# Kernel optimization log

Hardware: AMD Instinct MI355X
Metric: run time of the kernel (lower is better)

## Reference

```python
import jax, jax.numpy as jnp
import numpy as np

B = 2048
ENB = 16      # enb_cnt (beams)
RBG = 32      # rbg_cnt
MAXREQ = 50   # max_req
OBS_F = 400   # Requests features = 50*8
H = 1024
OUT = ENB * RBG * (MAXREQ + 1)  # 26112
IN = OBS_F + ENB * RBG + ENB * MAXREQ  # 1712


def _linear_init(key, fan_in, fan_out):
    kw, kb = jax.random.split(key)
    lim = 1.0 / np.sqrt(fan_in)
    W = jax.random.uniform(kw, (fan_in, fan_out), jnp.float32, -lim, lim)
    b = jax.random.uniform(kb, (fan_out,), jnp.float32, -lim, lim)
    return W, b


def setup_inputs() -> dict:
    key = jax.random.key(0)
    ks = jax.random.split(key, 6)
    obs = jax.random.normal(ks[0], (B, OBS_F), jnp.float32)
    rbgMap = jax.random.randint(ks[1], (B, ENB, RBG), 0, 2).astype(jnp.float32)
    invFlag = (jax.random.randint(ks[2], (B, ENB, MAXREQ), 0, 3) - 1).astype(jnp.float32)
    W1, b1 = _linear_init(ks[3], IN, H)
    W2, b2 = _linear_init(ks[4], H, H)
    W3, b3 = _linear_init(ks[5], H, OUT)
    return {"obs": obs, "rbgMap": rbgMap, "invFlag": invFlag,
            "W1": W1, "b1": b1, "W2": W2, "b2": b2, "W3": W3, "b3": b3}


def reference(obs, rbgMap, invFlag, W1, b1, W2, b2, W3, b3):
    Bt = obs.shape[0]
    rbg_flat = rbgMap.reshape(Bt, ENB * RBG)                      # [B, E*R]
    inv = invFlag.reshape(Bt, ENB, MAXREQ)
    # am1: invFlag broadcast per-rbg -> [B, E*R, MAXREQ]
    am1 = jnp.broadcast_to(inv[:, :, None, :], (Bt, ENB, RBG, MAXREQ)).reshape(Bt, ENB * RBG, MAXREQ)
    rbg_exp = rbg_flat[:, :, None]                                 # [B, E*R, 1]
    # vectorized form of the nested loops:
    #   where am1 == -1: -> 1 if rbg==0, 0 if rbg==1; else unchanged
    am1 = jnp.where(am1 == -1.0, jnp.where(rbg_exp == 0.0, 1.0, 0.0), am1)
    # prepend never-masked no-op action column, mask = nonzero
    amask = jnp.concatenate([jnp.zeros((Bt, ENB * RBG, 1), am1.dtype), am1], axis=2) != 0
    # dense MLP on concatenated observation
    inp = jnp.concatenate([obs, rbg_flat, invFlag.reshape(Bt, -1)], axis=1)  # [B, 1712]
    h = jnp.tanh(inp @ W1 + b1)
    h = jnp.tanh(h @ W2 + b2)
    logits = (h @ W3 + b3).reshape(Bt, ENB * RBG, MAXREQ + 1)
    logits = jnp.where(amask, -jnp.inf, logits)
    return logits
```

## Files before the change

kernel.cpp:

```cpp
#include <hip/hip_runtime.h>
#include <math.h>

#define B_    2048
#define OBSF_ 400
#define H_    1024
#define IN_   1712
#define INP_  1728
#define KS1_  54
#define KSH_  32
#define OUT_  26112
#define NCOL_ 51
#define MAXQ_ 50

#define NEG_BIG (-3.0e38f)

typedef __attribute__((ext_vector_type(4))) float  floatx4;
typedef __bf16 bf16x8 __attribute__((ext_vector_type(8)));

__device__ __forceinline__ unsigned short f2b(float v) {
    unsigned u = __float_as_uint(v);
    u += 0x7FFFu + ((u >> 16) & 1u);
    return (unsigned short)(u >> 16);
}


__global__ __launch_bounds__(256)
void pack_frag(const float* __restrict__ obs,
               const float* __restrict__ rbg,
               const float* __restrict__ inv,
               unsigned short* __restrict__ P) {
    const int tid = threadIdx.x;
    const int wave = tid >> 6, lane = tid & 63;
    const int cid = blockIdx.x * 4 + wave;
    const int ks = cid % KS1_, r16 = cid / KS1_;
    const int r = r16 * 16 + (lane & 15);
    const int kb = ks * 32 + (lane >> 4) * 8;
    __attribute__((aligned(16))) unsigned short tmp[8];
    #pragma unroll
    for (int j = 0; j < 8; j++) {
        int k = kb + j;
        float v = 0.0f;
        if (k < OBSF_)            v = obs[r * OBSF_ + k];
        else if (k < OBSF_ + 512) v = rbg[r * 512 + (k - OBSF_)];
        else if (k < IN_)         v = inv[r * 800 + (k - OBSF_ - 512)];
        tmp[j] = f2b(v);
    }
    *(uint4*)(P + ((size_t)(r16 * KS1_ + ks) * 64 + lane) * 8) = *(const uint4*)tmp;
}

__global__ __launch_bounds__(256)
void transpose_frag(const float* __restrict__ W, unsigned short* __restrict__ P,
                    int K, int N, int KS) {
    __shared__ float tile[32][129];
    const int n0 = blockIdx.x * 128, k0 = blockIdx.y * 32;
    const int tid = threadIdx.x;
    const int nn = tid & 127, kk0 = tid >> 7;
    #pragma unroll
    for (int i = 0; i < 16; i++) {
        int k = k0 + kk0 + i * 2;
        float v = 0.0f;
        if (k < K) v = W[(size_t)k * N + n0 + nn];
        tile[kk0 + i * 2][nn] = v;
    }
    __syncthreads();
    const int wave = tid >> 6, lane = tid & 63;
    const int i16 = lane & 15, q = lane >> 4;
    #pragma unroll
    for (int c2 = 0; c2 < 2; c2++) {
        const int c = wave * 2 + c2;
        __attribute__((aligned(16))) unsigned short tmp[8];
        #pragma unroll
        for (int j = 0; j < 8; j++) tmp[j] = f2b(tile[q * 8 + j][c * 16 + i16]);
        *(uint4*)(P + ((size_t)(((n0 >> 4) + c) * KS + (k0 >> 5)) * 64 + lane) * 8) =
            *(const uint4*)tmp;
    }
}

template<int MT, int NT, int KS, int EPI>
__global__ __launch_bounds__(256, 2)
void gemm_frag(const unsigned short* __restrict__ Ap,
               const unsigned short* __restrict__ Bp,
               const float* __restrict__ bias,
               void* __restrict__ outv,
               const float* __restrict__ rbg,
               const float* __restrict__ inv,
               int KSo) {
    const int tid = threadIdx.x;
    const int wave = tid >> 6, lane = tid & 63;
    const int wtm = blockIdx.y * 2 + (wave >> 1);
    const int wtn = blockIdx.x * 2 + (wave & 1);
    const int m16base = wtm * MT, n16base = wtn * NT;

    const unsigned short* pa = Ap + (size_t)m16base * KS * 512 + lane * 8;
    const unsigned short* pb = Bp + (size_t)n16base * KS * 512 + lane * 8;

    floatx4 acc[MT][NT];
    #pragma unroll
    for (int i = 0; i < MT; i++)
        #pragma unroll
        for (int j = 0; j < NT; j++) acc[i][j] = (floatx4){0.f, 0.f, 0.f, 0.f};

    bf16x8 a0[MT], b0[NT], a1[MT], b1[NT];
    #define LOADA(dst, ks_)                                                    \
        _Pragma("unroll") for (int mt = 0; mt < MT; mt++)                      \
            dst[mt] = *(const bf16x8*)(pa + (size_t)mt * KS * 512 + (ks_) * 512);
    #define LOADB(dst, ks_)                                                    \
        _Pragma("unroll") for (int nt = 0; nt < NT; nt++)                      \
            dst[nt] = *(const bf16x8*)(pb + (size_t)nt * KS * 512 + (ks_) * 512);
    #define MFMA(aa, bb)                                                       \
        _Pragma("unroll") for (int mt = 0; mt < MT; mt++)                      \
            _Pragma("unroll") for (int nt = 0; nt < NT; nt++)                  \
                acc[mt][nt] = __builtin_amdgcn_mfma_f32_16x16x32_bf16(         \
                    aa[mt], bb[nt], acc[mt][nt], 0, 0, 0);

    LOADA(a0, 0); LOADB(b0, 0);
    for (int ks = 0; ks < KS; ks += 2) {
        LOADA(a1, ks + 1); LOADB(b1, ks + 1);
        MFMA(a0, b0);
        int k2 = (ks + 2 < KS) ? ks + 2 : 0;
        LOADA(a0, k2); LOADB(b0, k2);
        MFMA(a1, b1);
    }
    #undef LOADA
    #undef LOADB
    #undef MFMA

    const int quad = lane >> 4;
    #pragma unroll
    for (int nt = 0; nt < NT; nt++) {
        const int col = (n16base + nt) * 16 + (lane & 15);
        const float bv = bias[col];
        unsigned short* Hp = (unsigned short*)outv;
        const int ko = col >> 5, kb = (col >> 3) & 3, kj = col & 7;
        #pragma unroll
        for (int mt = 0; mt < MT; mt++) {
            const int m16 = m16base + mt;
            #pragma unroll
            for (int r = 0; r < 4; r++) {
                const int mlo = quad * 4 + r;
                Hp[((size_t)(m16 * KSo + ko) * 64 + (mlo | (kb << 4))) * 8 + kj] =
                    f2b(tanhf(acc[mt][nt][r] + bv));
            }
        }
    }
}

typedef __attribute__((address_space(1))) const unsigned int gu32;
typedef __attribute__((address_space(3))) unsigned int su32;
__device__ __forceinline__ void async_copy16(unsigned short* l, const unsigned short* g) {
    __builtin_amdgcn_global_load_lds((gu32*)g, (su32*)l, 16, 0, 0);
}

template<int MT, int NT, int KS>
__global__ __launch_bounds__(256, 2)
void gemm_lds(const unsigned short* __restrict__ Ap,
              const unsigned short* __restrict__ Bp,
              const float* __restrict__ bias,
              float* __restrict__ C,
              const float* __restrict__ rbg,
              const float* __restrict__ inv) {
    constexpr int ACH = 2 * MT;
    constexpr int CH  = ACH + 2 * NT;
    constexpr int CPW = CH / 4;
    static_assert(CH % 4 == 0, "chunk count must split across 4 waves");
    static_assert(CPW == 4, "vmcnt literal below assumes CPW==4");
    static_assert(KS >= 5 && (KS - 2) % 3 == 0, "main loop unrolls by 3");
    __shared__ __align__(16) unsigned short lds[3][CH][512];

    const int tid  = threadIdx.x;
    const int wave = tid >> 6, lane = tid & 63;

    const int i = blockIdx.x;
    const int xcd = i & 7, j = i >> 3;
    const int g = xcd * 408 + j;
    const int panel = g >> 4;
    const int m     = g & 15;
    const int blk_m16 = m * ACH;
    const int blk_n16 = panel * 2 * NT;

    const int rg = wave >> 1, cg = wave & 1;
    const int m16base = blk_m16 + rg * MT;
    const int n16base = blk_n16 + cg * NT;

    const int chunk0 = wave * CPW;
    const unsigned short* gb[CPW];
    #pragma unroll
    for (int q = 0; q < CPW; q++) {
        const int c = chunk0 + q;
        gb[q] = (c < ACH ? Ap + (size_t)(blk_m16 + c) * KS * 512
                         : Bp + (size_t)(blk_n16 + (c - ACH)) * KS * 512)
                + lane * 8;
    }

    floatx4 acc[MT][NT];
    #pragma unroll
    for (int a = 0; a < MT; a++)
        #pragma unroll
        for (int b = 0; b < NT; b++) acc[a][b] = (floatx4){0.f, 0.f, 0.f, 0.f};

    #define STAGE(bufi, ksv) do {                                              \
        _Pragma("unroll")                                                      \
        for (int q = 0; q < CPW; q++)                                          \
            async_copy16(&lds[bufi][chunk0 + q][0], gb[q] + (size_t)(ksv) * 512); \
    } while (0)

    #define COMPUTE(bufi) do {                                                 \
        bf16x8 af[MT], bv[NT];                                                 \
        _Pragma("unroll")                                                      \
        for (int mt = 0; mt < MT; mt++)                                        \
            af[mt] = *(const bf16x8*)&lds[bufi][rg * MT + mt][lane * 8];       \
        _Pragma("unroll")                                                      \
        for (int nt = 0; nt < NT; nt++)                                        \
            bv[nt] = *(const bf16x8*)&lds[bufi][ACH + cg * NT + nt][lane * 8]; \
        __builtin_amdgcn_s_setprio(1);                                         \
        _Pragma("unroll")                                                      \
        for (int mt = 0; mt < MT; mt++)                                        \
            _Pragma("unroll")                                                  \
            for (int nt = 0; nt < NT; nt++)                                    \
                acc[mt][nt] = __builtin_amdgcn_mfma_f32_16x16x32_bf16(         \
                    af[mt], bv[nt], acc[mt][nt], 0, 0, 0);                     \
        __builtin_amdgcn_s_setprio(0);                                         \
    } while (0)

    #define STEP(CB, NB, tv) do {                                              \
        STAGE(NB, (tv) + 2);          \
        COMPUTE(CB);                                                           \
        asm volatile("s_waitcnt vmcnt(4)" ::: "memory");   \
        __builtin_amdgcn_s_barrier();                                          \
        asm volatile("" ::: "memory");                                         \
    } while (0)

    STAGE(0, 0);
    STAGE(1, 1);
    asm volatile("s_waitcnt vmcnt(4)" ::: "memory");
    __builtin_amdgcn_s_barrier();
    asm volatile("" ::: "memory");

    #pragma unroll 1
    for (int t = 0; t < KS - 2; t += 3) {
        STEP(0, 2, t);
        STEP(1, 0, t + 1);
        STEP(2, 1, t + 2);
    }
    COMPUTE(0);
    asm volatile("s_waitcnt vmcnt(0)" ::: "memory");
    __builtin_amdgcn_s_barrier();
    asm volatile("" ::: "memory");
    COMPUTE(1);
    #undef STEP
    #undef STAGE
    #undef COMPUTE

    const int quad = lane >> 4;
    #pragma unroll
    for (int nt = 0; nt < NT; nt++) {
        const int col = (n16base + nt) * 16 + (lane & 15);
        const float bvs = bias[col];
        const int jj = col / NCOL_;
        const int qq = col - jj * NCOL_;
        const int e  = jj >> 5;
        #pragma unroll
        for (int mt = 0; mt < MT; mt++) {
            const int row0 = (m16base + mt) * 16 + quad * 4;
            #pragma unroll
            for (int r = 0; r < 4; r++) {
                const int row = row0 + r;
                float v = acc[mt][nt][r] + bvs;
                if (qq > 0) {
                    float iv = inv[(size_t)row * 800 + e * MAXQ_ + (qq - 1)];
                    if (iv == 1.0f ||
                        (iv == -1.0f && rbg[(size_t)row * 512 + jj] == 0.0f))
                        v = NEG_BIG;
                }
                __builtin_nontemporal_store(v, &C[(size_t)row * OUT_ + col]);
            }
        }
    }
}

extern "C" void kernel_launch(void* const* d_in, const int* in_sizes, int n_in,
                              void* d_out, int out_size, void* d_ws, size_t ws_size,
                              hipStream_t stream) {
    const float* obs = (const float*)d_in[0];
    const float* rbg = (const float*)d_in[1];
    const float* inv = (const float*)d_in[2];
    const float* W1  = (const float*)d_in[3];
    const float* b1  = (const float*)d_in[4];
    const float* W2  = (const float*)d_in[5];
    const float* b2  = (const float*)d_in[6];
    const float* W3  = (const float*)d_in[7];
    const float* b3  = (const float*)d_in[8];
    float* out = (float*)d_out;

    char* ws = (char*)d_ws;
    unsigned short* inpP = (unsigned short*)ws;  ws += (size_t)B_ * INP_ * 2;
    unsigned short* W1P  = (unsigned short*)ws;  ws += (size_t)H_ * INP_ * 2;
    unsigned short* W2P  = (unsigned short*)ws;  ws += (size_t)H_ * H_ * 2;
    unsigned short* W3P  = (unsigned short*)ws;  ws += (size_t)OUT_ * H_ * 2;
    unsigned short* h1P  = (unsigned short*)ws;  ws += (size_t)B_ * H_ * 2;
    unsigned short* h2P  = (unsigned short*)ws;

    pack_frag<<<dim3(KS1_ * (B_ / 16) / 4), 256, 0, stream>>>(obs, rbg, inv, inpP);

    transpose_frag<<<dim3(H_ / 128, INP_ / 32), 256, 0, stream>>>(W1, W1P, IN_, H_, KS1_);
    transpose_frag<<<dim3(H_ / 128, H_ / 32),   256, 0, stream>>>(W2, W2P, H_, H_, KSH_);
    transpose_frag<<<dim3(OUT_ / 128, H_ / 32), 256, 0, stream>>>(W3, W3P, H_, OUT_, KSH_);

    gemm_frag<2, 2, KS1_, 0><<<dim3(H_ / 64, B_ / 64), 256, 0, stream>>>(
        inpP, W1P, b1, h1P, nullptr, nullptr, KSH_);
    gemm_frag<2, 2, KSH_, 0><<<dim3(H_ / 64, B_ / 64), 256, 0, stream>>>(
        h1P, W2P, b2, h2P, nullptr, nullptr, KSH_);
    gemm_lds<4, 4, KSH_><<<dim3(16 * (OUT_ / 128)), 256, 0, stream>>>(
        h2P, W3P, b3, out, rbg, inv);
}
```

Baseline: 577.1 us.

## Load B operand straight to registers, stage only A through LDS

The output GEMM kernel now feeds the B (weight) fragments from global memory directly into double-buffered registers, one k-step ahead. Only the A tiles still go through the triple-buffered LDS ring, which shrinks LDS per block, and the launch bounds are raised to three blocks per CU. The main loop is unrolled by six to rotate the register buffers, and the vmcnt waits are recounted for the extra loads. The aim is to cut LDS traffic and ds_reads for B and raise occupancy. The cost is that each B fragment is fetched twice from global/L2, once per row-group wave, and register pressure goes up.

```diff
diff --git a/kernel.cpp b/kernel.cpp
--- a/kernel.cpp
+++ b/kernel.cpp
@@ -152,7 +152,7 @@
 }
 
 template<int MT, int NT, int KS>
-__global__ __launch_bounds__(256, 2)
+__global__ __launch_bounds__(256, 3)
 void gemm_lds(const unsigned short* __restrict__ Ap,
               const unsigned short* __restrict__ Bp,
               const float* __restrict__ bias,
@@ -160,12 +160,10 @@
               const float* __restrict__ rbg,
               const float* __restrict__ inv) {
     constexpr int ACH = 2 * MT;
-    constexpr int CH  = ACH + 2 * NT;
-    constexpr int CPW = CH / 4;
-    static_assert(CH % 4 == 0, "chunk count must split across 4 waves");
-    static_assert(CPW == 4, "vmcnt literal below assumes CPW==4");
-    static_assert(KS >= 5 && (KS - 2) % 3 == 0, "main loop unrolls by 3");
-    __shared__ __align__(16) unsigned short lds[3][CH][512];
+    constexpr int CPW = ACH / 4;
+    static_assert(CPW == 2 && NT == 4, "vmcnt literals assume 2 stage + 4 B loads");
+    static_assert(KS % 6 == 2, "prologue 2 + 6k main + tail 2");
+    __shared__ __align__(16) unsigned short lds[3][ACH][512];
 
     const int tid  = threadIdx.x;
     const int wave = tid >> 6, lane = tid & 63;
@@ -182,73 +180,86 @@
     const int m16base = blk_m16 + rg * MT;
     const int n16base = blk_n16 + cg * NT;
 
-    const int chunk0 = wave * CPW;
-    const unsigned short* gb[CPW];
-    #pragma unroll
-    for (int q = 0; q < CPW; q++) {
-        const int c = chunk0 + q;
-        gb[q] = (c < ACH ? Ap + (size_t)(blk_m16 + c) * KS * 512
-                         : Bp + (size_t)(blk_n16 + (c - ACH)) * KS * 512)
-                + lane * 8;
-    }
+    const unsigned short* ga[CPW];
+    #pragma unroll
+    for (int q = 0; q < CPW; q++)
+        ga[q] = Ap + (size_t)(blk_m16 + wave * CPW + q) * KS * 512 + lane * 8;
+    const unsigned short* pb[NT];
+    #pragma unroll
+    for (int nt = 0; nt < NT; nt++)
+        pb[nt] = Bp + (size_t)(n16base + nt) * KS * 512 + lane * 8;
 
     floatx4 acc[MT][NT];
     #pragma unroll
     for (int a = 0; a < MT; a++)
         #pragma unroll
         for (int b = 0; b < NT; b++) acc[a][b] = (floatx4){0.f, 0.f, 0.f, 0.f};
+
+    bf16x8 bb0[NT], bb1[NT];
 
     #define STAGE(bufi, ksv) do {                                              \
         _Pragma("unroll")                                                      \
         for (int q = 0; q < CPW; q++)                                          \
-            async_copy16(&lds[bufi][chunk0 + q][0], gb[q] + (size_t)(ksv) * 512); \
+            async_copy16(&lds[bufi][wave * CPW + q][0],                        \
+                         ga[q] + (size_t)(ksv) * 512);                         \
     } while (0)
 
-    #define COMPUTE(bufi) do {                                                 \
-        bf16x8 af[MT], bv[NT];                                                 \
+    #define LOADB(dst, ksv) do {                                               \
+        _Pragma("unroll")                                                      \
+        for (int nt = 0; nt < NT; nt++)                                        \
+            dst[nt] = *(const bf16x8*)(pb[nt] + (size_t)(ksv) * 512);          \
+    } while (0)
+
+    #define COMPUTE(p3, B) do {                                                \
+        bf16x8 af[MT];                                                         \
         _Pragma("unroll")                                                      \
         for (int mt = 0; mt < MT; mt++)                                        \
-            af[mt] = *(const bf16x8*)&lds[bufi][rg * MT + mt][lane * 8];       \
-        _Pragma("unroll")                                                      \
-        for (int nt = 0; nt < NT; nt++)                                        \
-            bv[nt] = *(const bf16x8*)&lds[bufi][ACH + cg * NT + nt][lane * 8]; \
+            af[mt] = *(const bf16x8*)&lds[p3][rg * MT + mt][lane * 8];         \
         __builtin_amdgcn_s_setprio(1);                                         \
         _Pragma("unroll")                                                      \
         for (int mt = 0; mt < MT; mt++)                                        \
             _Pragma("unroll")                                                  \
             for (int nt = 0; nt < NT; nt++)                                    \
                 acc[mt][nt] = __builtin_amdgcn_mfma_f32_16x16x32_bf16(         \
-                    af[mt], bv[nt], acc[mt][nt], 0, 0, 0);                     \
+                    af[mt], B[nt], acc[mt][nt], 0, 0, 0);                      \
         __builtin_amdgcn_s_setprio(0);                                         \
     } while (0)
 
-    #define STEP(CB, NB, tv) do {                                              \
-        STAGE(NB, (tv) + 2);          \
-        COMPUTE(CB);                                                           \
-        asm volatile("s_waitcnt vmcnt(4)" ::: "memory");   \
+    #define STEP(P3, NB3, BCUR, BNXT, tv) do {                                 \
+        STAGE(NB3, (tv) + 2);                                                  \
+        LOADB(BNXT, (tv) + 1);                                                 \
+        COMPUTE(P3, BCUR);                                                     \
+        asm volatile("s_waitcnt vmcnt(6)" ::: "memory");                       \
         __builtin_amdgcn_s_barrier();                                          \
         asm volatile("" ::: "memory");                                         \
     } while (0)
 
     STAGE(0, 0);
     STAGE(1, 1);
+    LOADB(bb0, 0);
+    LOADB(bb1, 1);
+    asm volatile("s_waitcnt vmcnt(10)" ::: "memory");
+    __builtin_amdgcn_s_barrier();
+    asm volatile("" ::: "memory");
+
+    #pragma unroll 1
+    for (int t = 0; t < KS - 2; t += 6) {
+        STEP(0, 2, bb0, bb1, t);
+        STEP(1, 0, bb1, bb0, t + 1);
+        STEP(2, 1, bb0, bb1, t + 2);
+        STEP(0, 2, bb1, bb0, t + 3);
+        STEP(1, 0, bb0, bb1, t + 4);
+        STEP(2, 1, bb1, bb0, t + 5);
+    }
+    LOADB(bb1, KS - 1);
+    COMPUTE(0, bb0);
     asm volatile("s_waitcnt vmcnt(4)" ::: "memory");
     __builtin_amdgcn_s_barrier();
     asm volatile("" ::: "memory");
-
-    #pragma unroll 1
-    for (int t = 0; t < KS - 2; t += 3) {
-        STEP(0, 2, t);
-        STEP(1, 0, t + 1);
-        STEP(2, 1, t + 2);
-    }
-    COMPUTE(0);
-    asm volatile("s_waitcnt vmcnt(0)" ::: "memory");
-    __builtin_amdgcn_s_barrier();
-    asm volatile("" ::: "memory");
-    COMPUTE(1);
+    COMPUTE(1, bb1);
     #undef STEP
     #undef STAGE
+    #undef LOADB
     #undef COMPUTE
 
     const int quad = lane >> 4;
```

Result: slower. 597.5 us (+3.5%).
